# Kernel optimization log

Hardware: AMD Instinct MI355X
Metric: run time of the kernel (lower is better)

## Reference

```python
import jax, jax.numpy as jnp
import numpy as np

B, T, C, H = 1, 4096, 3072, 24
D = C // H  # 128


def _make_rope_freqs(t, d):
    # comfy-style rotation matrices: [t, d//2, 2, 2] with rows [[cos,-sin],[sin,cos]]
    half = d // 2
    inv = 1.0 / (10000.0 ** (np.arange(half, dtype=np.float64) / half))
    ang = np.arange(t, dtype=np.float64)[:, None] * inv[None, :]
    cos, sin = np.cos(ang), np.sin(ang)
    f = np.stack([np.stack([cos, -sin], -1), np.stack([sin, cos], -1)], -2)
    return jnp.asarray(f, jnp.float32)


def setup_inputs() -> dict:
    key = jax.random.key(0)
    ks = jax.random.split(key, 6)
    s = 0.02  # typical init scale
    x = jax.random.normal(ks[0], (B, T, C), jnp.float32)
    context = jax.random.normal(ks[1], (B, T, C), jnp.float32)
    Wq = jax.random.normal(ks[2], (C, C), jnp.float32) * s
    Wk = jax.random.normal(ks[3], (C, C), jnp.float32) * s
    Wv = jax.random.normal(ks[4], (C, C), jnp.float32) * s
    Wo = jax.random.normal(ks[5], (C, C), jnp.float32) * s
    freqs = _make_rope_freqs(T, D)  # [T, D//2, 2, 2]
    return {"x": x, "context": context, "freqs": freqs,
            "Wq": Wq, "Wk": Wk, "Wv": Wv, "Wo": Wo}


def _apply_rope(t, freqs):
    # t: [B, T, H, D]; freqs: [T, D//2, 2, 2]
    b, tt, h, d = t.shape
    tr = t.reshape(b, tt, h, d // 2, 1, 2)
    f = freqs[:, None]  # [T, 1, D//2, 2, 2] -> broadcast over B, H
    out = f[..., 0] * tr[..., 0] + f[..., 1] * tr[..., 1]  # [B,T,H,D//2,2]
    return out.reshape(b, tt, h, d)


def reference(x, context, freqs, Wq, Wk, Wv, Wo):
    # QKV projections (torch Linear: y = x @ W.T), kept in BTHD layout
    q = (x @ Wq.T).reshape(B, T, H, D)
    k = (context @ Wk.T).reshape(B, -1, H, D)
    v = (context @ Wv.T).reshape(B, -1, H, D)
    # RoPE on q and k
    q = _apply_rope(q, freqs)
    k = _apply_rope(k, freqs)
    # SDPA, non-causal, scale 1/sqrt(D) (jax expects BTNH layout)
    out = jax.nn.dot_product_attention(q, k, v)
    return out.reshape(B, T, C) @ Wo.T
```

## Files before the change

kernel.cpp:

```cpp
#include <hip/hip_runtime.h>
#include <hip/hip_bf16.h>

#define TT 4096
#define CC 3072
#define HH 24
#define DD 128

typedef __bf16 bf16;
typedef __attribute__((ext_vector_type(8))) __bf16 bf16x8;
typedef __attribute__((ext_vector_type(4))) __bf16 bf16x4;
typedef __attribute__((ext_vector_type(4))) float f32x4;
typedef __attribute__((ext_vector_type(16))) float f32x16;
typedef __attribute__((ext_vector_type(4))) unsigned uint32x4;

#define MFMA(a,b,c)   __builtin_amdgcn_mfma_f32_16x16x32_bf16((a),(b),(c),0,0,0)
#define MFMA32(a,b,c) __builtin_amdgcn_mfma_f32_32x32x16_bf16((a),(b),(c),0,0,0)

static __device__ __forceinline__ unsigned cvtpk(float lo, float hi) {
  unsigned r;
  asm("v_cvt_pk_bf16_f32 %0, %1, %2" : "=v"(r) : "v"(lo), "v"(hi));
  return r;
}
static __device__ __forceinline__ float max3f(float a, float b, float c) {
  float r;
  asm("v_max3_f32 %0, %1, %2, %3" : "=v"(r) : "v"(a), "v"(b), "v"(c));
  return r;
}
static __device__ __forceinline__ void plswap(unsigned &x, unsigned &y) {
  asm volatile("v_permlane32_swap_b32 %0, %1" : "+v"(x), "+v"(y));
}
static __device__ __forceinline__ void gl16(const bf16* g, bf16* l) {
  __builtin_amdgcn_global_load_lds(
      (const __attribute__((address_space(1))) unsigned int*)(g),
      (__attribute__((address_space(3))) unsigned int*)(l), 16, 0, 0);
}

__global__ __launch_bounds__(256)
void cvt_bf16(const float* __restrict__ in, bf16* __restrict__ out, int n8) {
  int i = blockIdx.x * 256 + threadIdx.x;
  const int stride = gridDim.x * 256;
  for (; i < n8; i += stride) {
    const float4* p = (const float4*)(in + (size_t)i * 8);
    float4 a = p[0], b = p[1];
    bf16x8 o;
    o[0]=(bf16)a.x; o[1]=(bf16)a.y; o[2]=(bf16)a.z; o[3]=(bf16)a.w;
    o[4]=(bf16)b.x; o[5]=(bf16)b.y; o[6]=(bf16)b.z; o[7]=(bf16)b.w;
    *(bf16x8*)(out + (size_t)i * 8) = o;
  }
}

template<int OBF>
__global__ __launch_bounds__(256, 2)
void gemm_bt(const bf16* __restrict__ A, const bf16* __restrict__ B,
             void* __restrict__ Cp, int M, int N, int K) {
  __shared__ bf16 As[128 * 32];
  __shared__ bf16 Bs[128 * 32];
  const int tid = threadIdx.x, lane = tid & 63, wid = tid >> 6;
  const int m0 = blockIdx.y * 128, n0 = blockIdx.x * 128;
  const int wr = (wid >> 1) * 64, wc = (wid & 1) * 64;
  const int r = lane & 15, g = lane >> 4;
  const int srow = lane >> 2, scol = (lane & 3) * 8;

  f32x4 acc[4][4] = {};
  const int NT = K >> 5;

  for (int kt = 0; kt < NT; ++kt) {
    const int kk = kt << 5;
    if (kt) __syncthreads();
    #pragma unroll
    for (int j = 0; j < 2; ++j) {
      const int base = (wid * 2 + j) * 16;
      gl16(A + (size_t)(m0 + base + srow) * K + kk + scol, As + base * 32);
      gl16(B + (size_t)(n0 + base + srow) * K + kk + scol, Bs + base * 32);
    }
    __syncthreads();

    bf16x8 af[4], bfr[4];
    #pragma unroll
    for (int m = 0; m < 4; ++m) af[m]  = *(const bf16x8*)&As[(wr + m*16 + r)*32 + g*8];
    #pragma unroll
    for (int n = 0; n < 4; ++n) bfr[n] = *(const bf16x8*)&Bs[(wc + n*16 + r)*32 + g*8];
    #pragma unroll
    for (int m = 0; m < 4; ++m)
      #pragma unroll
      for (int n = 0; n < 4; ++n)
        acc[m][n] = MFMA(af[m], bfr[n], acc[m][n]);
  }

  #pragma unroll
  for (int m = 0; m < 4; ++m)
    #pragma unroll
    for (int n = 0; n < 4; ++n) {
      const int col = n0 + wc + n*16 + r;
      #pragma unroll
      for (int j = 0; j < 4; ++j) {
        const int row = m0 + wr + m*16 + g*4 + j;
        float v = acc[m][n][j];
        if constexpr (OBF) ((bf16*)Cp)[(size_t)row*N + col] = (bf16)v;
        else               ((float*)Cp)[(size_t)row*N + col] = v;
      }
    }
}

template<int ABF, int OBF>
__global__ __launch_bounds__(256, 2)
void gemm_nt(const void* __restrict__ Ap, const float* __restrict__ Bp,
             void* __restrict__ Cp, int M, int N, int K) {
  __shared__ bf16 As[2][128][40];
  __shared__ bf16 Bs[2][128][40];
  const int tid = threadIdx.x;
  const int lane = tid & 63, wid = tid >> 6;
  const int m0 = blockIdx.y * 128, n0 = blockIdx.x * 128;
  const int wr = (wid >> 1) * 64, wc = (wid & 1) * 64;
  const int r = lane & 15, g = lane >> 4;
  const float* Af = (const float*)Ap;
  const bf16*  Ab = (const bf16*)Ap;

  f32x4 acc[4][4] = {};
  f32x4 pa[4], pb[4];
  bf16x8 qa[2];
  const int NT = K >> 5;

  auto load_tiles = [&](int kt) {
    const int kk = kt * 32;
    if constexpr (ABF) {
      #pragma unroll
      for (int j = 0; j < 2; ++j) {
        int c = tid + 256*j, row = c >> 2, kc = c & 3;
        qa[j] = *(const bf16x8*)(Ab + (size_t)(m0+row)*K + kk + kc*8);
      }
    } else {
      #pragma unroll
      for (int j = 0; j < 4; ++j) {
        int c = tid + 256*j, row = c >> 3, kc = c & 7;
        pa[j] = *(const f32x4*)(Af + (size_t)(m0+row)*K + kk + kc*4);
      }
    }
    #pragma unroll
    for (int j = 0; j < 4; ++j) {
      int c = tid + 256*j, row = c >> 3, kc = c & 7;
      pb[j] = *(const f32x4*)(Bp + (size_t)(n0+row)*K + kk + kc*4);
    }
  };
  auto write_tiles = [&](int buf) {
    if constexpr (ABF) {
      #pragma unroll
      for (int j = 0; j < 2; ++j) {
        int c = tid + 256*j, row = c >> 2, kc = c & 3;
        *(bf16x8*)&As[buf][row][kc*8] = qa[j];
      }
    } else {
      #pragma unroll
      for (int j = 0; j < 4; ++j) {
        int c = tid + 256*j, row = c >> 3, kc = c & 7;
        bf16x4 b;
        b[0]=(bf16)pa[j][0]; b[1]=(bf16)pa[j][1]; b[2]=(bf16)pa[j][2]; b[3]=(bf16)pa[j][3];
        *(bf16x4*)&As[buf][row][kc*4] = b;
      }
    }
    #pragma unroll
    for (int j = 0; j < 4; ++j) {
      int c = tid + 256*j, row = c >> 3, kc = c & 7;
      bf16x4 b;
      b[0]=(bf16)pb[j][0]; b[1]=(bf16)pb[j][1]; b[2]=(bf16)pb[j][2]; b[3]=(bf16)pb[j][3];
      *(bf16x4*)&Bs[buf][row][kc*4] = b;
    }
  };

  load_tiles(0);
  write_tiles(0);
  __syncthreads();
  for (int kt = 0; kt < NT; ++kt) {
    const int cur = kt & 1;
    if (kt + 1 < NT) load_tiles(kt + 1);
    bf16x8 af[4], bfr[4];
    #pragma unroll
    for (int m = 0; m < 4; ++m) af[m]  = *(const bf16x8*)&As[cur][wr + m*16 + r][g*8];
    #pragma unroll
    for (int n = 0; n < 4; ++n) bfr[n] = *(const bf16x8*)&Bs[cur][wc + n*16 + r][g*8];
    #pragma unroll
    for (int m = 0; m < 4; ++m)
      #pragma unroll
      for (int n = 0; n < 4; ++n)
        acc[m][n] = MFMA(af[m], bfr[n], acc[m][n]);
    if (kt + 1 < NT) write_tiles((kt + 1) & 1);
    __syncthreads();
  }
  #pragma unroll
  for (int m = 0; m < 4; ++m)
    #pragma unroll
    for (int n = 0; n < 4; ++n) {
      const int col = n0 + wc + n*16 + r;
      #pragma unroll
      for (int j = 0; j < 4; ++j) {
        const int row = m0 + wr + m*16 + g*4 + j;
        float v = acc[m][n][j];
        if constexpr (OBF) ((bf16*)Cp)[(size_t)row*N + col] = (bf16)v;
        else               ((float*)Cp)[(size_t)row*N + col] = v;
      }
    }
}

__global__ __launch_bounds__(256)
void rope_kernel(bf16* __restrict__ X, const float* __restrict__ F, float scale) {
  const int i = blockIdx.x * 256 + threadIdx.x;
  const size_t e8 = (size_t)i * 8;
  const int t  = (int)(e8 / CC);
  const int c  = (int)(e8 % CC);
  const int hc = c & (DD - 1);
  const float4* f = (const float4*)(F + (size_t)t*256 + (hc>>1)*4);
  bf16x8 v = *(const bf16x8*)(X + e8);
  bf16x8 o;
  #pragma unroll
  for (int p = 0; p < 4; ++p) {
    float x0 = (float)v[2*p], x1 = (float)v[2*p+1];
    float4 ff = f[p];
    o[2*p]   = (bf16)((ff.x*x0 + ff.y*x1) * scale);
    o[2*p+1] = (bf16)((ff.z*x0 + ff.w*x1) * scale);
  }
  *(bf16x8*)(X + e8) = o;
}

__global__ __launch_bounds__(256)
void transpose_v(const bf16* __restrict__ V, bf16* __restrict__ Vt) {
  __shared__ bf16 tile[64 * 128];
  const int t0 = blockIdx.x * 64, h = blockIdx.y;
  const int tid = threadIdx.x;
  #pragma unroll
  for (int j = 0; j < 4; ++j) {
    int c = tid + 256*j, t = c >> 4, c16 = c & 15;
    uint4 val = *(const uint4*)(V + (size_t)(t0+t)*CC + h*DD + c16*8);
    int sw = ((t & 7) ^ ((t >> 3) & 7)) << 4;
    *(uint4*)((char*)tile + t*256 + ((c16*16) ^ sw)) = val;
  }
  __syncthreads();
  #pragma unroll
  for (int j = 0; j < 4; ++j) {
    int c = tid + 256*j, d = c >> 3, c8 = c & 7;
    bf16x8 o;
    #pragma unroll
    for (int i = 0; i < 8; ++i) {
      int t = c8*8 + i;
      int sw = ((t & 7) ^ ((t >> 3) & 7)) << 4;
      o[i] = *(const bf16*)((char*)tile + t*256 + ((d*2) ^ sw));
    }
    *(bf16x8*)(Vt + (size_t)(h*DD + d)*TT + t0 + c8*8) = o;
  }
}

__global__ __launch_bounds__(256, 3)
void attn_kernel(const bf16* __restrict__ Q, const bf16* __restrict__ Kb,
                 const bf16* __restrict__ Vt, bf16* __restrict__ O) {
  __shared__ bf16 Ks[64 * 128];
  __shared__ bf16 Vs[64 * 128];

  const int tid = threadIdx.x, lane = tid & 63, wid = tid >> 6;
  const int c31 = lane & 31, g2 = lane >> 5;

  const int bid = blockIdx.x;
  const int fid = (bid & 7) * 96 + (bid >> 3);
  const int h = fid >> 5, qt = fid & 31;
  const int qrow = qt * 128 + wid * 32 + c31;

  bf16x8 aq[8];
  {
    const bf16* qp = Q + (size_t)qrow * CC + h * DD + g2 * 8;
    #pragma unroll
    for (int d0 = 0; d0 < 8; ++d0) aq[d0] = *(const bf16x8*)(qp + d0 * 16);
  }

  float m_ = -1e30f, l_ = 0.f;
  f32x16 o_[4] = {};

  auto stage = [&](int kv0) {
    uint4 kr[4], vr4[4];
    #pragma unroll
    for (int j = 0; j < 4; ++j) {
      int cc = tid + 256*j, row = cc >> 4, c16 = cc & 15;
      kr[j] = *(const uint4*)(Kb + (size_t)(kv0 + row) * CC + h * DD + c16 * 8);
    }
    #pragma unroll
    for (int j = 0; j < 4; ++j) {
      int cc = tid + 256*j, row = cc >> 3, c8 = cc & 7;
      vr4[j] = *(const uint4*)(Vt + (size_t)(h * DD + row) * TT + kv0 + c8 * 8);
    }
    #pragma unroll
    for (int j = 0; j < 4; ++j) {
      int cc = tid + 256*j, row = cc >> 4, c16 = cc & 15;
      *(uint4*)((char*)Ks + row * 256 + ((c16 * 16) ^ ((row & 15) << 4))) = kr[j];
    }
    #pragma unroll
    for (int j = 0; j < 4; ++j) {
      int cc = tid + 256*j, row = cc >> 3, c8 = cc & 7;
      const int R = row >> 1, ch = (row & 1) * 8 + c8;
      *(uint4*)((char*)Vs + R * 256 + ((ch * 16) ^ ((R & 15) << 4))) = vr4[j];
    }
  };

  const int NT = TT / 64;
  for (int t = 0; t < NT; ++t) {
    if (t) __syncthreads();
    stage(t * 64);
    __syncthreads();

    f32x16 s[2] = {};
    __builtin_amdgcn_s_setprio(1);
    #pragma unroll
    for (int d0 = 0; d0 < 8; ++d0) {
      #pragma unroll
      for (int tt = 0; tt < 2; ++tt) {
        const int kvr = tt * 32 + c31;
        bf16x8 ak = *(const bf16x8*)((const char*)Ks + kvr * 256 +
                                     ((d0 * 32 + g2 * 16) ^ ((kvr & 15) << 4)));
        s[tt] = MFMA32(ak, aq[d0], s[tt]);
      }
    }
    __builtin_amdgcn_s_setprio(0);

    float mx = fmaxf(s[0][0], s[0][1]);
    #pragma unroll
    for (int i = 2; i < 16; i += 2) mx = max3f(mx, s[0][i], s[0][i+1]);
    #pragma unroll
    for (int i = 0; i < 16; i += 2) mx = max3f(mx, s[1][i], s[1][i+1]);
    mx = fmaxf(mx, __shfl_xor(mx, 32, 64));
    if (!__all(mx <= m_ + 8.f)) {
      float mn = fmaxf(m_, mx);
      float al = __builtin_amdgcn_exp2f(m_ - mn);
      l_ *= al;
      #pragma unroll
      for (int d0 = 0; d0 < 4; ++d0) o_[d0] *= al;
      m_ = mn;
    }

    unsigned w0[8], w1[8];
    float rs = 0.f;
    #pragma unroll
    for (int jj = 0; jj < 8; ++jj) {
      float a0 = __builtin_amdgcn_exp2f(s[0][2*jj] - m_);
      float b0 = __builtin_amdgcn_exp2f(s[0][2*jj+1] - m_);
      float a1 = __builtin_amdgcn_exp2f(s[1][2*jj] - m_);
      float b1 = __builtin_amdgcn_exp2f(s[1][2*jj+1] - m_);
      rs += (a0 + b0) + (a1 + b1);
      w0[jj] = cvtpk(a0, b0);
      w1[jj] = cvtpk(a1, b1);
    }
    rs += __shfl_xor(rs, 32, 64);
    l_ += rs;

    bf16x8 pb[4];
    #pragma unroll
    for (int t2 = 0; t2 < 4; ++t2) {
      const int jA = (t2 & 1) * 4;
      unsigned x0, y0, x1, y1;
      if (t2 < 2) { x0 = w0[jA]; y0 = w0[jA+2]; x1 = w0[jA+1]; y1 = w0[jA+3]; }
      else        { x0 = w1[jA]; y0 = w1[jA+2]; x1 = w1[jA+1]; y1 = w1[jA+3]; }
      plswap(x0, y0);
      plswap(x1, y1);
      uint32x4 uu; uu[0] = x0; uu[1] = x1; uu[2] = y0; uu[3] = y1;
      pb[t2] = __builtin_bit_cast(bf16x8, uu);
    }

    __builtin_amdgcn_s_setprio(1);
    #pragma unroll
    for (int d0 = 0; d0 < 4; ++d0) {
      const int dd = d0 * 32 + c31;
      const int R = dd >> 1, chb = (c31 & 1) * 8;
      #pragma unroll
      for (int t2 = 0; t2 < 4; ++t2) {
        const int ch = chb + t2 * 2 + g2;
        bf16x8 av = *(const bf16x8*)((const char*)Vs + R * 256 +
                                     ((ch * 16) ^ ((R & 15) << 4)));
        o_[d0] = MFMA32(av, pb[t2], o_[d0]);
      }
    }
    __builtin_amdgcn_s_setprio(0);
  }

  const float inv = 1.f / l_;
  bf16* orow = O + (size_t)qrow * CC + h * DD;
  #pragma unroll
  for (int d0 = 0; d0 < 4; ++d0)
    #pragma unroll
    for (int q4 = 0; q4 < 4; ++q4) {
      uint2 val;
      val.x = cvtpk(o_[d0][q4*4 + 0] * inv, o_[d0][q4*4 + 1] * inv);
      val.y = cvtpk(o_[d0][q4*4 + 2] * inv, o_[d0][q4*4 + 3] * inv);
      *(uint2*)(orow + d0*32 + q4*8 + g2*4) = val;
    }
}

extern "C" void kernel_launch(void* const* d_in, const int* in_sizes, int n_in,
                              void* d_out, int out_size, void* d_ws, size_t ws_size,
                              hipStream_t stream) {
  const float* x   = (const float*)d_in[0];
  const float* ctx = (const float*)d_in[1];
  const float* fr  = (const float*)d_in[2];
  const float* Wq  = (const float*)d_in[3];
  const float* Wk  = (const float*)d_in[4];
  const float* Wv  = (const float*)d_in[5];
  const float* Wo  = (const float*)d_in[6];
  float* out = (float*)d_out;
  char* ws = (char*)d_ws;

  const size_t SZ  = (size_t)TT * CC * sizeof(bf16);
  const size_t WSZ = (size_t)CC * CC * sizeof(bf16);
  bf16* Qb  = (bf16*)(ws);
  bf16* Kbf = (bf16*)(ws + SZ);
  bf16* Vb  = (bf16*)(ws + 2*SZ);
  bf16* Vtb = (bf16*)(ws + 3*SZ);
  bf16* Ob  = Vb;

  const int rblocks = (TT*CC/8)/256;
  const float QSCALE = 0.12751743314942355f;

  const size_t NEED = 5*SZ + 3*WSZ;
  if (ws_size >= NEED) {
    bf16* xb   = Vtb;
    bf16* ctxb = (bf16*)(ws + 4*SZ);
    bf16* Wqb  = (bf16*)(ws + 5*SZ);
    bf16* Wkb  = (bf16*)(ws + 5*SZ + WSZ);
    bf16* Wvb  = (bf16*)(ws + 5*SZ + 2*WSZ);
    bf16* Wob  = Wqb;

    cvt_bf16<<<2048, 256, 0, stream>>>(x,   xb,   TT*CC/8);
    cvt_bf16<<<2048, 256, 0, stream>>>(ctx, ctxb, TT*CC/8);
    cvt_bf16<<<2048, 256, 0, stream>>>(Wq,  Wqb,  CC*CC/8);
    cvt_bf16<<<2048, 256, 0, stream>>>(Wk,  Wkb,  CC*CC/8);
    cvt_bf16<<<2048, 256, 0, stream>>>(Wv,  Wvb,  CC*CC/8);

    dim3 gg(CC/128, TT/128);
    gemm_bt<1><<<gg, 256, 0, stream>>>(xb,   Wqb, Qb,  TT, CC, CC);
    gemm_bt<1><<<gg, 256, 0, stream>>>(ctxb, Wkb, Kbf, TT, CC, CC);
    gemm_bt<1><<<gg, 256, 0, stream>>>(ctxb, Wvb, Vb,  TT, CC, CC);

    rope_kernel<<<rblocks, 256, 0, stream>>>(Qb,  fr, QSCALE);
    rope_kernel<<<rblocks, 256, 0, stream>>>(Kbf, fr, 1.0f);

    transpose_v<<<dim3(TT/64, HH), 256, 0, stream>>>(Vb, Vtb);
    cvt_bf16<<<2048, 256, 0, stream>>>(Wo, Wob, CC*CC/8);
    attn_kernel<<<dim3(768), 256, 0, stream>>>(Qb, Kbf, Vtb, Ob);

    gemm_bt<0><<<gg, 256, 0, stream>>>(Ob, Wob, out, TT, CC, CC);
  } else {
    dim3 gg(CC/128, TT/128);
    gemm_nt<0,1><<<gg, 256, 0, stream>>>(x,   Wq, Qb,  TT, CC, CC);
    gemm_nt<0,1><<<gg, 256, 0, stream>>>(ctx, Wk, Kbf, TT, CC, CC);
    gemm_nt<0,1><<<gg, 256, 0, stream>>>(ctx, Wv, Vb,  TT, CC, CC);
    rope_kernel<<<rblocks, 256, 0, stream>>>(Qb,  fr, QSCALE);
    rope_kernel<<<rblocks, 256, 0, stream>>>(Kbf, fr, 1.0f);
    transpose_v<<<dim3(TT/64, HH), 256, 0, stream>>>(Vb, Vtb);
    attn_kernel<<<dim3(768), 256, 0, stream>>>(Qb, Kbf, Vtb, Ob);
    gemm_nt<1,0><<<gg, 256, 0, stream>>>(Ob, Wo, out, TT, CC, CC);
  }
}
```

Baseline: 739.4 us.

## Split attention KV range in two with fp32 partials and merge kernel

```diff
diff --git a/kernel.cpp b/kernel.cpp
--- a/kernel.cpp
+++ b/kernel.cpp
@@ -248,9 +248,11 @@
   }
 }
 
+template<int SPLIT>
 __global__ __launch_bounds__(256, 3)
 void attn_kernel(const bf16* __restrict__ Q, const bf16* __restrict__ Kb,
-                 const bf16* __restrict__ Vt, bf16* __restrict__ O) {
+                 const bf16* __restrict__ Vt, void* __restrict__ Outp,
+                 float* __restrict__ ml) {
   __shared__ bf16 Ks[64 * 128];
   __shared__ bf16 Vs[64 * 128];
 
@@ -258,8 +260,16 @@
   const int c31 = lane & 31, g2 = lane >> 5;
 
   const int bid = blockIdx.x;
-  const int fid = (bid & 7) * 96 + (bid >> 3);
-  const int h = fid >> 5, qt = fid & 31;
+  int h, qt, half, kvbase, NT;
+  if constexpr (SPLIT) {
+    const int fid = (bid & 7) * 192 + (bid >> 3);
+    h = fid >> 6; half = (fid >> 5) & 1; qt = fid & 31;
+    kvbase = half * (TT / 2); NT = TT / 128;
+  } else {
+    const int fid = (bid & 7) * 96 + (bid >> 3);
+    h = fid >> 5; half = 0; qt = fid & 31;
+    kvbase = 0; NT = TT / 64;
+  }
   const int qrow = qt * 128 + wid * 32 + c31;
 
   bf16x8 aq[8];
@@ -297,10 +307,9 @@
     }
   };
 
-  const int NT = TT / 64;
   for (int t = 0; t < NT; ++t) {
     if (t) __syncthreads();
-    stage(t * 64);
+    stage(kvbase + t * 64);
     __syncthreads();
 
     f32x16 s[2] = {};
@@ -376,17 +385,60 @@
     __builtin_amdgcn_s_setprio(0);
   }
 
-  const float inv = 1.f / l_;
-  bf16* orow = O + (size_t)qrow * CC + h * DD;
-  #pragma unroll
-  for (int d0 = 0; d0 < 4; ++d0)
-    #pragma unroll
-    for (int q4 = 0; q4 < 4; ++q4) {
-      uint2 val;
-      val.x = cvtpk(o_[d0][q4*4 + 0] * inv, o_[d0][q4*4 + 1] * inv);
-      val.y = cvtpk(o_[d0][q4*4 + 2] * inv, o_[d0][q4*4 + 3] * inv);
-      *(uint2*)(orow + d0*32 + q4*8 + g2*4) = val;
-    }
+  if constexpr (SPLIT) {
+    float* orow = (float*)Outp + ((size_t)half * TT * CC) + (size_t)qrow * CC + h * DD;
+    #pragma unroll
+    for (int d0 = 0; d0 < 4; ++d0)
+      #pragma unroll
+      for (int q4 = 0; q4 < 4; ++q4) {
+        float4 v;
+        v.x = o_[d0][q4*4 + 0]; v.y = o_[d0][q4*4 + 1];
+        v.z = o_[d0][q4*4 + 2]; v.w = o_[d0][q4*4 + 3];
+        *(float4*)(orow + d0*32 + q4*8 + g2*4) = v;
+      }
+    if (g2 == 0) {
+      float2 v; v.x = m_; v.y = l_;
+      *(float2*)(ml + 2 * ((size_t)(half * HH + h) * TT + qrow)) = v;
+    }
+  } else {
+    const float inv = 1.f / l_;
+    bf16* orow = (bf16*)Outp + (size_t)qrow * CC + h * DD;
+    #pragma unroll
+    for (int d0 = 0; d0 < 4; ++d0)
+      #pragma unroll
+      for (int q4 = 0; q4 < 4; ++q4) {
+        uint2 val;
+        val.x = cvtpk(o_[d0][q4*4 + 0] * inv, o_[d0][q4*4 + 1] * inv);
+        val.y = cvtpk(o_[d0][q4*4 + 2] * inv, o_[d0][q4*4 + 3] * inv);
+        *(uint2*)(orow + d0*32 + q4*8 + g2*4) = val;
+      }
+  }
+}
+
+__global__ __launch_bounds__(256)
+void merge_o(const float* __restrict__ Op, const float* __restrict__ ml,
+             bf16* __restrict__ O) {
+  const int i = blockIdx.x * 256 + threadIdx.x;
+  const size_t e8 = (size_t)i * 8;
+  const int row = (int)(e8 / CC);
+  const int c   = (int)(e8 % CC);
+  const int h   = c >> 7;
+  float2 a = *(const float2*)(ml + 2 * ((size_t)h * TT + row));
+  float2 b = *(const float2*)(ml + 2 * ((size_t)(HH + h) * TT + row));
+  const float m  = fmaxf(a.x, b.x);
+  const float a1 = __builtin_amdgcn_exp2f(a.x - m);
+  const float a2 = __builtin_amdgcn_exp2f(b.x - m);
+  const float inv = 1.f / (a.y * a1 + b.y * a2);
+  const float4* p1 = (const float4*)(Op + e8);
+  const float4* p2 = (const float4*)(Op + (size_t)TT * CC + e8);
+  float4 x1 = p1[0], y1 = p1[1], x2 = p2[0], y2 = p2[1];
+  uint2 lo, hi;
+  lo.x = cvtpk((x1.x*a1 + x2.x*a2) * inv, (x1.y*a1 + x2.y*a2) * inv);
+  lo.y = cvtpk((x1.z*a1 + x2.z*a2) * inv, (x1.w*a1 + x2.w*a2) * inv);
+  hi.x = cvtpk((y1.x*a1 + y2.x*a2) * inv, (y1.y*a1 + y2.y*a2) * inv);
+  hi.y = cvtpk((y1.z*a1 + y2.z*a2) * inv, (y1.w*a1 + y2.w*a2) * inv);
+  *(uint2*)(O + e8) = lo;
+  *(uint2*)(O + e8 + 4) = hi;
 }
 
 extern "C" void kernel_launch(void* const* d_in, const int* in_sizes, int n_in,
@@ -404,6 +456,7 @@
 
   const size_t SZ  = (size_t)TT * CC * sizeof(bf16);
   const size_t WSZ = (size_t)CC * CC * sizeof(bf16);
+  const size_t FSZ = (size_t)TT * CC * sizeof(float);
   bf16* Qb  = (bf16*)(ws);
   bf16* Kbf = (bf16*)(ws + SZ);
   bf16* Vb  = (bf16*)(ws + 2*SZ);
@@ -413,7 +466,8 @@
   const int rblocks = (TT*CC/8)/256;
   const float QSCALE = 0.12751743314942355f;
 
-  const size_t NEED = 5*SZ + 3*WSZ;
+  const size_t NEED  = 5*SZ + 3*WSZ;
+  const size_t NEED2 = NEED + 2*FSZ + (size_t)2*HH*TT*2*sizeof(float);
   if (ws_size >= NEED) {
     bf16* xb   = Vtb;
     bf16* ctxb = (bf16*)(ws + 4*SZ);
@@ -438,7 +492,15 @@
 
     transpose_v<<<dim3(TT/64, HH), 256, 0, stream>>>(Vb, Vtb);
     cvt_bf16<<<2048, 256, 0, stream>>>(Wo, Wob, CC*CC/8);
-    attn_kernel<<<dim3(768), 256, 0, stream>>>(Qb, Kbf, Vtb, Ob);
+
+    if (ws_size >= NEED2) {
+      float* Op  = (float*)(ws + NEED);
+      float* mlp = (float*)(ws + NEED + 2*FSZ);
+      attn_kernel<1><<<dim3(1536), 256, 0, stream>>>(Qb, Kbf, Vtb, Op, mlp);
+      merge_o<<<rblocks, 256, 0, stream>>>(Op, mlp, Ob);
+    } else {
+      attn_kernel<0><<<dim3(768), 256, 0, stream>>>(Qb, Kbf, Vtb, Ob, nullptr);
+    }
 
     gemm_bt<0><<<gg, 256, 0, stream>>>(Ob, Wob, out, TT, CC, CC);
   } else {
@@ -449,7 +511,7 @@
     rope_kernel<<<rblocks, 256, 0, stream>>>(Qb,  fr, QSCALE);
     rope_kernel<<<rblocks, 256, 0, stream>>>(Kbf, fr, 1.0f);
     transpose_v<<<dim3(TT/64, HH), 256, 0, stream>>>(Vb, Vtb);
-    attn_kernel<<<dim3(768), 256, 0, stream>>>(Qb, Kbf, Vtb, Ob);
+    attn_kernel<0><<<dim3(768), 256, 0, stream>>>(Qb, Kbf, Vtb, Ob, nullptr);
     gemm_nt<1,0><<<gg, 256, 0, stream>>>(Ob, Wo, out, TT, CC, CC);
   }
 }
```

Result: slower. 874.6 us (+18.3%).

## Replace bf16 GEMM with 256x256 tile, 8-wave, double-buffered pipelined kernel

Applied to the files above, without the earlier changes.

```diff
diff --git a/kernel.cpp b/kernel.cpp
--- a/kernel.cpp
+++ b/kernel.cpp
@@ -50,52 +50,134 @@
 }
 
 template<int OBF>
-__global__ __launch_bounds__(256, 2)
-void gemm_bt(const bf16* __restrict__ A, const bf16* __restrict__ B,
-             void* __restrict__ Cp, int M, int N, int K) {
-  __shared__ bf16 As[128 * 32];
-  __shared__ bf16 Bs[128 * 32];
+__global__ __launch_bounds__(512, 2)
+void gemm8(const bf16* __restrict__ A, const bf16* __restrict__ B,
+           void* __restrict__ Cp, int M, int N, int K) {
+  __shared__ bf16 As[2][2][256][32];
+  __shared__ bf16 Bs[2][2][256][32];
   const int tid = threadIdx.x, lane = tid & 63, wid = tid >> 6;
-  const int m0 = blockIdx.y * 128, n0 = blockIdx.x * 128;
-  const int wr = (wid >> 1) * 64, wc = (wid & 1) * 64;
+
+  const int bid = blockIdx.x;
+  const int fid = (bid & 7) * 24 + (bid >> 3);
+  const int NBX = N >> 8;
+  const int bx = fid % NBX, by = fid / NBX;
+  const int m0 = by * 256, n0 = bx * 256;
+  const int wm = wid >> 2, wn = wid & 3;
   const int r = lane & 15, g = lane >> 4;
   const int srow = lane >> 2, scol = (lane & 3) * 8;
 
-  f32x4 acc[4][4] = {};
-  const int NT = K >> 5;
+  f32x4 acc[8][4] = {};
+  const int NT = K >> 6;
+
+  auto issueA = [&](int kt, int tb) {
+    const int kk = kt << 6;
+    #pragma unroll
+    for (int kh = 0; kh < 2; ++kh)
+      #pragma unroll
+      for (int j = 0; j < 2; ++j) {
+        const int st = wid * 2 + j;
+        gl16(A + (size_t)(m0 + st*16 + srow) * K + kk + kh*32 + scol,
+             &As[tb][kh][st*16][0]);
+      }
+  };
+  auto issueB = [&](int kt, int tb) {
+    const int kk = kt << 6;
+    #pragma unroll
+    for (int kh = 0; kh < 2; ++kh)
+      #pragma unroll
+      for (int j = 0; j < 2; ++j) {
+        const int st = wid * 2 + j;
+        gl16(B + (size_t)(n0 + st*16 + srow) * K + kk + kh*32 + scol,
+             &Bs[tb][kh][st*16][0]);
+      }
+  };
+
+  issueA(0, 0); issueB(0, 0);
+  asm volatile("s_waitcnt vmcnt(0)" ::: "memory");
+  __builtin_amdgcn_s_barrier();
+
+  bf16x8 af[4][2];
+  bf16x8 bq[2][2][2];
 
   for (int kt = 0; kt < NT; ++kt) {
-    const int kk = kt << 5;
-    if (kt) __syncthreads();
-    #pragma unroll
-    for (int j = 0; j < 2; ++j) {
-      const int base = (wid * 2 + j) * 16;
-      gl16(A + (size_t)(m0 + base + srow) * K + kk + scol, As + base * 32);
-      gl16(B + (size_t)(n0 + base + srow) * K + kk + scol, Bs + base * 32);
-    }
-    __syncthreads();
-
-    bf16x8 af[4], bfr[4];
-    #pragma unroll
-    for (int m = 0; m < 4; ++m) af[m]  = *(const bf16x8*)&As[(wr + m*16 + r)*32 + g*8];
-    #pragma unroll
-    for (int n = 0; n < 4; ++n) bfr[n] = *(const bf16x8*)&Bs[(wc + n*16 + r)*32 + g*8];
-    #pragma unroll
-    for (int m = 0; m < 4; ++m)
-      #pragma unroll
-      for (int n = 0; n < 4; ++n)
-        acc[m][n] = MFMA(af[m], bfr[n], acc[m][n]);
+    const int b = kt & 1;
+    #pragma unroll
+    for (int mf = 0; mf < 4; ++mf)
+      #pragma unroll
+      for (int ks = 0; ks < 2; ++ks)
+        af[mf][ks] = *(const bf16x8*)&As[b][ks][wm*128 + mf*16 + r][g*8];
+    #pragma unroll
+    for (int nf = 0; nf < 2; ++nf)
+      #pragma unroll
+      for (int ks = 0; ks < 2; ++ks)
+        bq[0][nf][ks] = *(const bf16x8*)&Bs[b][ks][wn*64 + nf*16 + r][g*8];
+    if (kt + 1 < NT) issueA(kt + 1, b ^ 1);
+    __builtin_amdgcn_s_barrier();
+    __builtin_amdgcn_s_setprio(1);
+    #pragma unroll
+    for (int mf = 0; mf < 4; ++mf)
+      #pragma unroll
+      for (int nf = 0; nf < 2; ++nf)
+        #pragma unroll
+        for (int ks = 0; ks < 2; ++ks)
+          acc[mf][nf] = MFMA(af[mf][ks], bq[0][nf][ks], acc[mf][nf]);
+    __builtin_amdgcn_s_setprio(0);
+    __builtin_amdgcn_s_barrier();
+    #pragma unroll
+    for (int nf = 0; nf < 2; ++nf)
+      #pragma unroll
+      for (int ks = 0; ks < 2; ++ks)
+        bq[1][nf][ks] = *(const bf16x8*)&Bs[b][ks][wn*64 + 32 + nf*16 + r][g*8];
+    if (kt + 1 < NT) issueB(kt + 1, b ^ 1);
+    __builtin_amdgcn_s_barrier();
+    __builtin_amdgcn_s_setprio(1);
+    #pragma unroll
+    for (int mf = 0; mf < 4; ++mf)
+      #pragma unroll
+      for (int nf = 0; nf < 2; ++nf)
+        #pragma unroll
+        for (int ks = 0; ks < 2; ++ks)
+          acc[mf][2+nf] = MFMA(af[mf][ks], bq[1][nf][ks], acc[mf][2+nf]);
+    __builtin_amdgcn_s_setprio(0);
+    __builtin_amdgcn_s_barrier();
+    #pragma unroll
+    for (int mf = 0; mf < 4; ++mf)
+      #pragma unroll
+      for (int ks = 0; ks < 2; ++ks)
+        af[mf][ks] = *(const bf16x8*)&As[b][ks][wm*128 + 64 + mf*16 + r][g*8];
+    __builtin_amdgcn_s_barrier();
+    __builtin_amdgcn_s_setprio(1);
+    #pragma unroll
+    for (int mf = 0; mf < 4; ++mf)
+      #pragma unroll
+      for (int nf = 0; nf < 2; ++nf)
+        #pragma unroll
+        for (int ks = 0; ks < 2; ++ks)
+          acc[4+mf][2+nf] = MFMA(af[mf][ks], bq[1][nf][ks], acc[4+mf][2+nf]);
+    __builtin_amdgcn_s_setprio(0);
+    __builtin_amdgcn_s_barrier();
+    __builtin_amdgcn_s_setprio(1);
+    #pragma unroll
+    for (int mf = 0; mf < 4; ++mf)
+      #pragma unroll
+      for (int nf = 0; nf < 2; ++nf)
+        #pragma unroll
+        for (int ks = 0; ks < 2; ++ks)
+          acc[4+mf][nf] = MFMA(af[mf][ks], bq[0][nf][ks], acc[4+mf][nf]);
+    __builtin_amdgcn_s_setprio(0);
+    asm volatile("s_waitcnt vmcnt(0)" ::: "memory");
+    __builtin_amdgcn_s_barrier();
   }
 
   #pragma unroll
-  for (int m = 0; m < 4; ++m)
-    #pragma unroll
-    for (int n = 0; n < 4; ++n) {
-      const int col = n0 + wc + n*16 + r;
+  for (int mf = 0; mf < 8; ++mf)
+    #pragma unroll
+    for (int nf = 0; nf < 4; ++nf) {
+      const int col = n0 + wn*64 + nf*16 + r;
       #pragma unroll
       for (int j = 0; j < 4; ++j) {
-        const int row = m0 + wr + m*16 + g*4 + j;
-        float v = acc[m][n][j];
+        const int row = m0 + wm*128 + mf*16 + g*4 + j;
+        float v = acc[mf][nf][j];
         if constexpr (OBF) ((bf16*)Cp)[(size_t)row*N + col] = (bf16)v;
         else               ((float*)Cp)[(size_t)row*N + col] = v;
       }
@@ -428,10 +510,10 @@
     cvt_bf16<<<2048, 256, 0, stream>>>(Wk,  Wkb,  CC*CC/8);
     cvt_bf16<<<2048, 256, 0, stream>>>(Wv,  Wvb,  CC*CC/8);
 
-    dim3 gg(CC/128, TT/128);
-    gemm_bt<1><<<gg, 256, 0, stream>>>(xb,   Wqb, Qb,  TT, CC, CC);
-    gemm_bt<1><<<gg, 256, 0, stream>>>(ctxb, Wkb, Kbf, TT, CC, CC);
-    gemm_bt<1><<<gg, 256, 0, stream>>>(ctxb, Wvb, Vb,  TT, CC, CC);
+    const int g8 = (TT/256) * (CC/256);
+    gemm8<1><<<g8, 512, 0, stream>>>(xb,   Wqb, Qb,  TT, CC, CC);
+    gemm8<1><<<g8, 512, 0, stream>>>(ctxb, Wkb, Kbf, TT, CC, CC);
+    gemm8<1><<<g8, 512, 0, stream>>>(ctxb, Wvb, Vb,  TT, CC, CC);
 
     rope_kernel<<<rblocks, 256, 0, stream>>>(Qb,  fr, QSCALE);
     rope_kernel<<<rblocks, 256, 0, stream>>>(Kbf, fr, 1.0f);
@@ -440,7 +522,7 @@
     cvt_bf16<<<2048, 256, 0, stream>>>(Wo, Wob, CC*CC/8);
     attn_kernel<<<dim3(768), 256, 0, stream>>>(Qb, Kbf, Vtb, Ob);
 
-    gemm_bt<0><<<gg, 256, 0, stream>>>(Ob, Wob, out, TT, CC, CC);
+    gemm8<0><<<g8, 512, 0, stream>>>(Ob, Wob, out, TT, CC, CC);
   } else {
     dim3 gg(CC/128, TT/128);
     gemm_nt<0,1><<<gg, 256, 0, stream>>>(x,   Wq, Qb,  TT, CC, CC);
```

New measurement: 787.9 us. +6.6%, slower.
